# Kernel tuning notes

Hardware: AMD Instinct MI355X
Metric: run time of the kernel (lower is better)

## Reference

```python
import jax, jax.numpy as jnp
import numpy as np
import math

EPS = 1e-5  # BatchNorm eps; eval mode with running_mean=0, running_var=1


def maxpool(x, k, p):
    return jax.lax.reduce_window(x, -jnp.inf, jax.lax.max,
                                 (1, 1, k, k), (1, 1, 1, 1),
                                 ((0, 0), (0, 0), (p, p), (p, p)))


def conv1x1(x, w, b=None):
    # x: [B,Cin,H,W], w: [Cout,Cin]
    y = jnp.einsum('oi,bihw->bohw', w, x)
    if b is not None:
        y = y + b[None, :, None, None]
    return y


def bn_eval(x, g, b):
    scale = g / jnp.sqrt(1.0 + EPS)
    return x * scale[None, :, None, None] + b[None, :, None, None]


def setup_inputs() -> dict:
    B, C, H, W = 2, 64, 80, 80
    c1, c2, c3 = 21, 21, 22
    ch = 32  # C//2
    ks = jax.random.split(jax.random.key(0), 16)
    s = 0.05
    inp = {
        'x': jax.random.normal(ks[0], (B, C, H, W), jnp.float32),
        'q1_w': jax.random.normal(ks[1], (c1, c1), jnp.float32) * s,
        'q1_g': jnp.ones((c1,), jnp.float32),
        'q1_b': jnp.zeros((c1,), jnp.float32),
        'q2_w': jax.random.normal(ks[2], (c2, c2), jnp.float32) * s,
        'q2_g': jnp.ones((c2,), jnp.float32),
        'q2_b': jnp.zeros((c2,), jnp.float32),
        'q3_w': jax.random.normal(ks[3], (c3, c3), jnp.float32) * s,
        'q3_g': jnp.ones((c3,), jnp.float32),
        'q3_b': jnp.zeros((c3,), jnp.float32),
        'k_hf_w': jax.random.normal(ks[4], (ch, C), jnp.float32) * s,
        'k_hf_b': jnp.zeros((ch,), jnp.float32),
        'k_lf_w': jax.random.normal(ks[5], (C - ch, C), jnp.float32) * s,
        'k_lf_b': jnp.zeros((C - ch,), jnp.float32),
        'k_fuse_w': jax.random.normal(ks[6], (C, C), jnp.float32) * s,
        'k_fuse_b': jnp.zeros((C,), jnp.float32),
        'v_bn_g': jnp.ones((C,), jnp.float32),
        'v_bn_b': jnp.zeros((C,), jnp.float32),
        'v_w': jax.random.normal(ks[7], (C, C), jnp.float32) * s,
        'v_b': jnp.zeros((C,), jnp.float32),
        'out_w': jax.random.normal(ks[8], (C, C), jnp.float32) * s,
        'out_b': jnp.zeros((C,), jnp.float32),
    }
    return inp


def reference(x, q1_w, q1_g, q1_b, q2_w, q2_g, q2_b, q3_w, q3_g, q3_b,
              k_hf_w, k_hf_b, k_lf_w, k_lf_b, k_fuse_w, k_fuse_b,
              v_bn_g, v_bn_b, v_w, v_b, out_w, out_b):
    B, C, H, W = x.shape
    N = H * W
    c1 = q1_w.shape[0]
    c2 = q2_w.shape[0]
    # Q: ThreeGroupConvQ (split -> 1x1 conv (no bias) -> BN -> ReLU -> concat)
    x1, x2, x3 = jnp.split(x, [c1, c1 + c2], axis=1)
    y1 = jax.nn.relu(bn_eval(conv1x1(x1, q1_w), q1_g, q1_b))
    y2 = jax.nn.relu(bn_eval(conv1x1(x2, q2_w), q2_g, q2_b))
    y3 = jax.nn.relu(bn_eval(conv1x1(x3, q3_w), q3_g, q3_b))
    Q = jnp.concatenate([y1, y2, y3], axis=1)
    # K: ThermalStructureExtractor
    p3 = maxpool(x, 3, 1)
    p5 = maxpool(x, 5, 2)
    low = (p3 + p5) * 0.5
    high = conv1x1(x - low, k_hf_w, k_hf_b)
    lowp = conv1x1(low, k_lf_w, k_lf_b)
    K = conv1x1(jnp.concatenate([high, lowp], axis=1), k_fuse_w, k_fuse_b)
    # V: BN -> 1x1 conv
    V = conv1x1(bn_eval(x, v_bn_g, v_bn_b), v_w, v_b)
    # attention over N = H*W spatial tokens, channel features
    Qc = Q.reshape(B, C, N)
    Kc = K.reshape(B, C, N)
    Vc = V.reshape(B, C, N)
    attn = jax.nn.softmax(
        jnp.einsum('bcn,bcm->bnm', Qc, Kc) / math.sqrt(C), axis=-1)  # [B,N,N]
    out = jnp.einsum('bnm,bcm->bcn', attn, Vc).reshape(B, C, H, W)
    return conv1x1(out, out_w, out_b) + x
```

## Files before the change

### kernel.cpp

```cpp
#include <hip/hip_runtime.h>
#include <hip/hip_bf16.h>


#define BATCH 2
#define CH 64
#define HH 80
#define WW 80
#define NN 6400
#define NT 100
#define KS 10
#define KTPS (NT/KS)
#define EPSV 1e-5f
#define NEGBIG (-1e30f)
#define LOG2E8 0.18033688f
#define VSP 65

typedef __hip_bfloat16 bf16;
typedef __attribute__((ext_vector_type(8))) short short8;
typedef __attribute__((ext_vector_type(4))) float f4;
#define MFMA16 __builtin_amdgcn_mfma_f32_16x16x32_bf16

__device__ __forceinline__ float b2f(bf16 v){ return __bfloat162float(v); }
__device__ __forceinline__ bf16 f2b(float v){ return __float2bfloat16(v); }
__device__ __forceinline__ ushort f2bu(float v){ return ((__hip_bfloat16_raw)__float2bfloat16(v)).x; }
__device__ __forceinline__ float bu2f(ushort u){
  union { unsigned int i; float f; } w; w.i = ((unsigned int)u) << 16; return w.f;
}
__device__ __forceinline__ unsigned pkbf(float a, float b){
  union { __hip_bfloat162 h2; unsigned u; } cv;
  cv.h2 = __float22bfloat162_rn(make_float2(a, b));
  return cv.u;
}
__device__ __forceinline__ float fexp2(float x){
#if __has_builtin(__builtin_amdgcn_exp2f)
  return __builtin_amdgcn_exp2f(x);
#else
  return exp2f(x);
#endif
}
__device__ __forceinline__ int swz(int row, int colb){
  return row*128 + (colb ^ ((row & 7) << 4));
}

#define OFF_BIAS 0
#define OFF_WH_B 768
#define OFF_LOW_B (768 + 32768)
#define OFF_Q_B   (OFF_LOW_B + BATCH*CH*NN*2)
#define OFF_K_B   (OFF_Q_B   + BATCH*CH*NN*2)
#define OFF_V_B   (OFF_K_B   + BATCH*CH*NN*2)
#define OFF_P_B   (OFF_V_B   + BATCH*CH*NN*2)
#define OFF_ML_B  (OFF_P_B   + BATCH*NT*KS*4096*2)

__global__ __launch_bounds__(256) void setup_fold(
    const float* __restrict__ q1w, const float* __restrict__ q1g, const float* __restrict__ q1b,
    const float* __restrict__ q2w, const float* __restrict__ q2g, const float* __restrict__ q2b,
    const float* __restrict__ q3w, const float* __restrict__ q3g, const float* __restrict__ q3b,
    const float* __restrict__ khw, const float* __restrict__ khb,
    const float* __restrict__ klw, const float* __restrict__ klb,
    const float* __restrict__ kfw, const float* __restrict__ kfb,
    const float* __restrict__ vg,  const float* __restrict__ vbnb,
    const float* __restrict__ vw,  const float* __restrict__ vb,
    const float* __restrict__ outw,
    float* __restrict__ biasf, bf16* __restrict__ wh)
{
  __shared__ __align__(16) float skf[4096];
  __shared__ __align__(16) float skh[2048];
  __shared__ __align__(16) float skl[2048];
  __shared__ __align__(16) float sow[4096];
  __shared__ __align__(16) float svw[4096];
  __shared__ float sbv[64];

  int tid = threadIdx.x;
  int blk = blockIdx.x;
  #pragma unroll
  for (int i = 0; i < 4; ++i) {
    *(float4*)&skf[(i*256 + tid)*4] = *(const float4*)&kfw[(i*256 + tid)*4];
    *(float4*)&sow[(i*256 + tid)*4] = *(const float4*)&outw[(i*256 + tid)*4];
    *(float4*)&svw[(i*256 + tid)*4] = *(const float4*)&vw[(i*256 + tid)*4];
  }
  #pragma unroll
  for (int i = 0; i < 2; ++i) {
    *(float4*)&skh[(i*256 + tid)*4] = *(const float4*)&khw[(i*256 + tid)*4];
    *(float4*)&skl[(i*256 + tid)*4] = *(const float4*)&klw[(i*256 + tid)*4];
  }
  __syncthreads();

  float rs = rsqrtf(1.0f + EPSV);
  if (tid < 64) {
    int j = tid;
    float bvo = vb[j];
    for (int ci2 = 0; ci2 < 64; ++ci2) bvo += svw[j*64 + ci2] * vbnb[ci2];
    sbv[j] = bvo;
  }

  bf16* wq   = wh;
  bf16* wvp  = wh + 4096;
  bf16* wa1  = wh + 8192;
  bf16* wa2m = wh + 12288;

  int t = blk*256 + tid;
  int ci = t & 63, co = t >> 6;
  int o = ci*64 + co;

  float w = 0.f, g;
  if (co < 21)      { g = q1g[co];    w = (ci < 21)              ? q1w[co*21 + ci]            : 0.f; }
  else if (co < 42) { g = q2g[co-21]; w = (ci >= 21 && ci < 42)  ? q2w[(co-21)*21 + (ci-21)]  : 0.f; }
  else              { g = q3g[co-42]; w = (ci >= 42)             ? q3w[(co-42)*22 + (ci-42)]  : 0.f; }
  wq[o] = f2b(w * g * rs * LOG2E8);

  float a1 = 0.f, a2 = 0.f;
  #pragma unroll
  for (int j = 0; j < 32; ++j) {
    a1 += skf[co*64 + j]      * skh[j*64 + ci];
    a2 += skf[co*64 + 32 + j] * skl[j*64 + ci];
  }
  wa1[o]  = f2b(a1);
  wa2m[o] = f2b(a2 - a1);

  float av = 0.f;
  #pragma unroll
  for (int j = 0; j < 64; ++j)
    av += sow[co*64 + j] * svw[j*64 + ci];
  wvp[o] = f2b(av * vg[ci] * rs);

  if (blk == 0 && tid < 64) {
    int c2 = tid;
    float bq;
    if (c2 < 21)      bq = q1b[c2];
    else if (c2 < 42) bq = q2b[c2-21];
    else              bq = q3b[c2-42];
    biasf[c2] = bq * LOG2E8;
    float bk = kfb[c2];
    #pragma unroll
    for (int j = 0; j < 32; ++j) {
      bk += skf[c2*64 + j]      * khb[j];
      bk += skf[c2*64 + 32 + j] * klb[j];
    }
    biasf[64 + c2] = bk;
    float bvp = 0.f;
    #pragma unroll
    for (int j = 0; j < 64; ++j) bvp += sow[c2*64 + j] * sbv[j];
    biasf[128 + c2] = bvp;
  }
}

__global__ __launch_bounds__(256) void pool_low(const float* __restrict__ x,
                                                bf16* __restrict__ lowg)
{
  int t4 = (blockIdx.x*256 + threadIdx.x)*4;
  int bc = t4 / NN; int n = t4 % NN;
  int h = n / WW, w0 = n % WW;
  const float* p = x + bc*NN;
  float m5[4], m3[4];
  #pragma unroll
  for (int j=0;j<4;++j){ m5[j]=NEGBIG; m3[j]=NEGBIG; }
  #pragma unroll
  for (int dh = -2; dh <= 2; ++dh) {
    int hh = h + dh; if (hh < 0 || hh >= HH) continue;
    float r[12];
    const float* row = p + hh*WW;
    if (w0 >= 4)      { float4 a = *(const float4*)&row[w0-4]; r[0]=a.x;r[1]=a.y;r[2]=a.z;r[3]=a.w; }
    else              { r[0]=NEGBIG;r[1]=NEGBIG;r[2]=NEGBIG;r[3]=NEGBIG; }
    { float4 a = *(const float4*)&row[w0]; r[4]=a.x;r[5]=a.y;r[6]=a.z;r[7]=a.w; }
    if (w0 + 7 < WW)  { float4 a = *(const float4*)&row[w0+4]; r[8]=a.x;r[9]=a.y;r[10]=a.z;r[11]=a.w; }
    else              { r[8]=NEGBIG;r[9]=NEGBIG;r[10]=NEGBIG;r[11]=NEGBIG; }
    bool in3 = (dh >= -1 && dh <= 1);
    #pragma unroll
    for (int j=0;j<4;++j) {
      float v3 = fmaxf(fmaxf(r[3+j], r[4+j]), r[5+j]);
      float v5 = fmaxf(fmaxf(r[2+j], v3), r[6+j]);
      m5[j] = fmaxf(m5[j], v5);
      if (in3) m3[j] = fmaxf(m3[j], v3);
    }
  }
  ushort4 o;
  o.x = f2bu(0.5f*(m3[0]+m5[0]));
  o.y = f2bu(0.5f*(m3[1]+m5[1]));
  o.z = f2bu(0.5f*(m3[2]+m5[2]));
  o.w = f2bu(0.5f*(m3[3]+m5[3]));
  *(ushort4*)&lowg[t4] = o;
}

__global__ __launch_bounds__(256) void qkv_kernel(
    const float* __restrict__ x, const float* __restrict__ biasf,
    const bf16* __restrict__ wh, const bf16* __restrict__ lowg,
    bf16* __restrict__ qgT, bf16* __restrict__ kgT, bf16* __restrict__ vgc)
{
  __shared__ __align__(16) float xs[64*32];
  __shared__ __align__(16) float lows[64*32];
  __shared__ __align__(16) bf16  wbuf[16384];
  __shared__ ushort vs[64*VSP];
  __shared__ float bias[192];

  int tid = threadIdx.x;
  int blk = blockIdx.x;
  int b = blk / (NT*2);
  int rem = blk % (NT*2);
  int tile = rem >> 1, half = rem & 1;
  int n0 = tile*64 + half*32;

  #pragma unroll
  for (int i = 0; i < 8; ++i) {
    int e = i*256 + tid; int c = e >> 5, p = e & 31;
    xs[c*32 + p]   = x[(b*CH + c)*NN + n0 + p];
    lows[c*32 + p] = b2f(lowg[(b*CH + c)*NN + n0 + p]);
  }
  #pragma unroll
  for (int i = 0; i < 16; ++i)
    ((uint2*)wbuf)[i*256 + tid] = ((const uint2*)wh)[i*256 + tid];
  if (tid < 192) bias[tid] = biasf[tid];
  __syncthreads();

  int co = tid & 63, pg = tid >> 6;
  const bf16* wq   = wbuf;
  const bf16* wvp  = wbuf + 4096;
  const bf16* wa1  = wbuf + 8192;
  const bf16* wa2m = wbuf + 12288;

  {
    float bq = bias[co];
    float4 a0 = make_float4(bq,bq,bq,bq), a1v = a0;
    for (int ci = 0; ci < 64; ++ci) {
      float wv = b2f(wq[ci*64 + co]);
      float4 x0 = *(const float4*)&xs[ci*32 + pg*8];
      float4 x1 = *(const float4*)&xs[ci*32 + pg*8 + 4];
      a0.x += wv*x0.x; a0.y += wv*x0.y; a0.z += wv*x0.z; a0.w += wv*x0.w;
      a1v.x += wv*x1.x; a1v.y += wv*x1.y; a1v.z += wv*x1.z; a1v.w += wv*x1.w;
    }
    float q8[8] = {a0.x,a0.y,a0.z,a0.w,a1v.x,a1v.y,a1v.z,a1v.w};
    #pragma unroll
    for (int j=0;j<8;++j)
      qgT[(size_t)(b*NN + n0 + pg*8 + j)*64 + co] = f2b(fmaxf(q8[j], 0.f));
  }
  {
    float bv = bias[128 + co];
    float4 a0 = make_float4(bv,bv,bv,bv), a1v = a0;
    for (int ci = 0; ci < 64; ++ci) {
      float wv = b2f(wvp[ci*64 + co]);
      float4 x0 = *(const float4*)&xs[ci*32 + pg*8];
      float4 x1 = *(const float4*)&xs[ci*32 + pg*8 + 4];
      a0.x += wv*x0.x; a0.y += wv*x0.y; a0.z += wv*x0.z; a0.w += wv*x0.w;
      a1v.x += wv*x1.x; a1v.y += wv*x1.y; a1v.z += wv*x1.z; a1v.w += wv*x1.w;
    }
    float v8[8] = {a0.x,a0.y,a0.z,a0.w,a1v.x,a1v.y,a1v.z,a1v.w};
    #pragma unroll
    for (int j=0;j<8;++j)
      vs[co*VSP + pg*8 + j] = f2bu(v8[j]);
  }
  __syncthreads();
  {
    int c = tid >> 2, cb = (tid & 3)*8;
    ushort u[8];
    #pragma unroll
    for (int j=0;j<8;++j) u[j] = vs[c*VSP + cb + j];
    uint4 pk;
    pk.x = (uint)u[0] | ((uint)u[1] << 16);
    pk.y = (uint)u[2] | ((uint)u[3] << 16);
    pk.z = (uint)u[4] | ((uint)u[5] << 16);
    pk.w = (uint)u[6] | ((uint)u[7] << 16);
    *(uint4*)&vgc[(size_t)(b*CH + c)*NN + n0 + cb] = pk;
  }
  {
    float bk = bias[64 + co];
    float4 a0 = make_float4(bk,bk,bk,bk), a1v = a0;
    for (int ci = 0; ci < 64; ++ci) {
      float w1 = b2f(wa1[ci*64 + co]);
      float w2 = b2f(wa2m[ci*64 + co]);
      float4 x0 = *(const float4*)&xs[ci*32 + pg*8];
      float4 x1 = *(const float4*)&xs[ci*32 + pg*8 + 4];
      float4 l0 = *(const float4*)&lows[ci*32 + pg*8];
      float4 l1 = *(const float4*)&lows[ci*32 + pg*8 + 4];
      a0.x += w1*x0.x + w2*l0.x; a0.y += w1*x0.y + w2*l0.y;
      a0.z += w1*x0.z + w2*l0.z; a0.w += w1*x0.w + w2*l0.w;
      a1v.x += w1*x1.x + w2*l1.x; a1v.y += w1*x1.y + w2*l1.y;
      a1v.z += w1*x1.z + w2*l1.z; a1v.w += w1*x1.w + w2*l1.w;
    }
    float k8[8] = {a0.x,a0.y,a0.z,a0.w,a1v.x,a1v.y,a1v.z,a1v.w};
    #pragma unroll
    for (int j=0;j<8;++j)
      kgT[(size_t)(b*NN + n0 + pg*8 + j)*64 + co] = f2b(k8[j]);
  }
}

__global__ __launch_bounds__(256, 2) void attn_partial(
    const bf16* __restrict__ qgT, const bf16* __restrict__ kgT, const bf16* __restrict__ vgc,
    ushort* __restrict__ part, float* __restrict__ pml)
{
  __shared__ __align__(16) char smem[32768];
  __shared__ float lred[256];

  int tid = threadIdx.x;
  int blk = blockIdx.x;
  int b = blk / (NT*KS);
  int rem = blk % (NT*KS);
  int tile = rem / KS, split = rem % KS;
  int n0 = tile*64;
  int wv = tid >> 6, lane = tid & 63, ln = lane & 15, quad = lane >> 4;
  int mbase = split*KTPS*64;

  int r0 = tid >> 3,         c0 = (tid & 7)*8;
  int r1 = 32 + (tid >> 3),  c1 = (tid & 7)*8;

  {
    uint4 qa = *(const uint4*)&qgT[(size_t)(b*NN + n0 + r0)*64 + c0];
    uint4 qb = *(const uint4*)&qgT[(size_t)(b*NN + n0 + r1)*64 + c1];
    *(uint4*)(smem + swz(r0, c0*2)) = qa;
    *(uint4*)(smem + swz(r1, c1*2)) = qb;
  }
  __syncthreads();
  short8 bq00 = *(const short8*)(smem + swz( 0*16 + ln, quad*16));
  short8 bq01 = *(const short8*)(smem + swz( 0*16 + ln, 64 + quad*16));
  short8 bq10 = *(const short8*)(smem + swz( 1*16 + ln, quad*16));
  short8 bq11 = *(const short8*)(smem + swz( 1*16 + ln, 64 + quad*16));
  short8 bq20 = *(const short8*)(smem + swz( 2*16 + ln, quad*16));
  short8 bq21 = *(const short8*)(smem + swz( 2*16 + ln, 64 + quad*16));
  short8 bq30 = *(const short8*)(smem + swz( 3*16 + ln, quad*16));
  short8 bq31 = *(const short8*)(smem + swz( 3*16 + ln, 64 + quad*16));
  {
    uint4 va = *(const uint4*)&vgc[(size_t)(b*CH + r0)*NN + mbase + c0];
    uint4 vb4 = *(const uint4*)&vgc[(size_t)(b*CH + r1)*NN + mbase + c1];
    *(uint4*)(smem + 16384 + swz(r0, c0*2)) = va;
    *(uint4*)(smem + 16384 + swz(r1, c1*2)) = vb4;
  }
  const bf16* kb = kgT + (size_t)(b*NN + mbase + wv*16 + ln)*64;
  short8 ak0 = *(const short8*)&kb[quad*8];
  short8 ak1 = *(const short8*)&kb[32 + quad*8];
  __syncthreads();

  f4 accO0 = (f4){0.f,0.f,0.f,0.f};
  f4 accO1 = (f4){0.f,0.f,0.f,0.f};
  f4 accO2 = (f4){0.f,0.f,0.f,0.f};
  f4 accO3 = (f4){0.f,0.f,0.f,0.f};
  float lacc0 = 0.f, lacc1 = 0.f, lacc2 = 0.f, lacc3 = 0.f;

  uint4 vr0, vr1;
  short8 an0, an1;
  for (int kt = 0; kt < KTPS; ++kt) {
    const int po = (kt & 1) * 8192;
    const int vo = 16384 + (kt & 1) * 8192;
    {
      int ktn = (kt + 1 < KTPS) ? kt + 1 : kt;
      int m1 = mbase + ktn*64;
      vr0 = *(const uint4*)&vgc[(size_t)(b*CH + r0)*NN + m1 + c0];
      vr1 = *(const uint4*)&vgc[(size_t)(b*CH + r1)*NN + m1 + c1];
      an0 = *(const short8*)&kb[(size_t)ktn*4096 + quad*8];
      an1 = *(const short8*)&kb[(size_t)ktn*4096 + 32 + quad*8];
    }

    f4 accS0, accS1, accS2, accS3;
    {
      f4 z = (f4){0.f,0.f,0.f,0.f};
      z = MFMA16(ak0, bq00, z, 0, 0, 0);
      accS0 = MFMA16(ak1, bq01, z, 0, 0, 0);
    }
    {
      f4 z = (f4){0.f,0.f,0.f,0.f};
      z = MFMA16(ak0, bq10, z, 0, 0, 0);
      accS1 = MFMA16(ak1, bq11, z, 0, 0, 0);
    }
    {
      f4 z = (f4){0.f,0.f,0.f,0.f};
      z = MFMA16(ak0, bq20, z, 0, 0, 0);
      accS2 = MFMA16(ak1, bq21, z, 0, 0, 0);
    }
    {
      f4 z = (f4){0.f,0.f,0.f,0.f};
      z = MFMA16(ak0, bq30, z, 0, 0, 0);
      accS3 = MFMA16(ak1, bq31, z, 0, 0, 0);
    }
    {
      float p0 = fexp2(accS0[0]), p1 = fexp2(accS0[1]);
      float p2 = fexp2(accS0[2]), p3 = fexp2(accS0[3]);
      lacc0 += (p0 + p1) + (p2 + p3);
      uint2 pk; pk.x = pkbf(p0, p1); pk.y = pkbf(p2, p3);
      *(uint2*)(smem + po + swz(0*16 + ln, wv*32 + quad*8)) = pk;
    }
    {
      float p0 = fexp2(accS1[0]), p1 = fexp2(accS1[1]);
      float p2 = fexp2(accS1[2]), p3 = fexp2(accS1[3]);
      lacc1 += (p0 + p1) + (p2 + p3);
      uint2 pk; pk.x = pkbf(p0, p1); pk.y = pkbf(p2, p3);
      *(uint2*)(smem + po + swz(1*16 + ln, wv*32 + quad*8)) = pk;
    }
    {
      float p0 = fexp2(accS2[0]), p1 = fexp2(accS2[1]);
      float p2 = fexp2(accS2[2]), p3 = fexp2(accS2[3]);
      lacc2 += (p0 + p1) + (p2 + p3);
      uint2 pk; pk.x = pkbf(p0, p1); pk.y = pkbf(p2, p3);
      *(uint2*)(smem + po + swz(2*16 + ln, wv*32 + quad*8)) = pk;
    }
    {
      float p0 = fexp2(accS3[0]), p1 = fexp2(accS3[1]);
      float p2 = fexp2(accS3[2]), p3 = fexp2(accS3[3]);
      lacc3 += (p0 + p1) + (p2 + p3);
      uint2 pk; pk.x = pkbf(p0, p1); pk.y = pkbf(p2, p3);
      *(uint2*)(smem + po + swz(3*16 + ln, wv*32 + quad*8)) = pk;
    }
    __syncthreads();

    short8 ap0 = *(const short8*)(smem + po + swz(wv*16 + ln, quad*16));
    short8 ap1 = *(const short8*)(smem + po + swz(wv*16 + ln, 64 + quad*16));
    {
      short8 bv0 = *(const short8*)(smem + vo + swz(0*16 + ln, quad*16));
      short8 bv1 = *(const short8*)(smem + vo + swz(0*16 + ln, 64 + quad*16));
      accO0 = MFMA16(ap0, bv0, accO0, 0, 0, 0);
      accO0 = MFMA16(ap1, bv1, accO0, 0, 0, 0);
    }
    {
      short8 bv0 = *(const short8*)(smem + vo + swz(1*16 + ln, quad*16));
      short8 bv1 = *(const short8*)(smem + vo + swz(1*16 + ln, 64 + quad*16));
      accO1 = MFMA16(ap0, bv0, accO1, 0, 0, 0);
      accO1 = MFMA16(ap1, bv1, accO1, 0, 0, 0);
    }
    {
      short8 bv0 = *(const short8*)(smem + vo + swz(2*16 + ln, quad*16));
      short8 bv1 = *(const short8*)(smem + vo + swz(2*16 + ln, 64 + quad*16));
      accO2 = MFMA16(ap0, bv0, accO2, 0, 0, 0);
      accO2 = MFMA16(ap1, bv1, accO2, 0, 0, 0);
    }
    {
      short8 bv0 = *(const short8*)(smem + vo + swz(3*16 + ln, quad*16));
      short8 bv1 = *(const short8*)(smem + vo + swz(3*16 + ln, 64 + quad*16));
      accO3 = MFMA16(ap0, bv0, accO3, 0, 0, 0);
      accO3 = MFMA16(ap1, bv1, accO3, 0, 0, 0);
    }
    if (kt + 1 < KTPS) {
      int vn = 16384 + ((kt+1) & 1) * 8192;
      *(uint4*)(smem + vn + swz(r0, c0*2)) = vr0;
      *(uint4*)(smem + vn + swz(r1, c1*2)) = vr1;
    }
    ak0 = an0; ak1 = an1;
  }

  size_t pbase = ((size_t)(b*NT + tile)*KS + split)*4096;
  ushort* pp = part + pbase;
  {
    uint2 pk; pk.x = pkbf(accO0[0], accO0[1]); pk.y = pkbf(accO0[2], accO0[3]);
    *(uint2*)&pp[(0*16 + ln)*64 + wv*16 + quad*4] = pk;
  }
  {
    uint2 pk; pk.x = pkbf(accO1[0], accO1[1]); pk.y = pkbf(accO1[2], accO1[3]);
    *(uint2*)&pp[(1*16 + ln)*64 + wv*16 + quad*4] = pk;
  }
  {
    uint2 pk; pk.x = pkbf(accO2[0], accO2[1]); pk.y = pkbf(accO2[2], accO2[3]);
    *(uint2*)&pp[(2*16 + ln)*64 + wv*16 + quad*4] = pk;
  }
  {
    uint2 pk; pk.x = pkbf(accO3[0], accO3[1]); pk.y = pkbf(accO3[2], accO3[3]);
    *(uint2*)&pp[(3*16 + ln)*64 + wv*16 + quad*4] = pk;
  }
  {
    float s = lacc0;
    s += __shfl_xor(s, 16); s += __shfl_xor(s, 32);
    if (quad == 0) lred[wv*64 + 0*16 + ln] = s;
  }
  {
    float s = lacc1;
    s += __shfl_xor(s, 16); s += __shfl_xor(s, 32);
    if (quad == 0) lred[wv*64 + 1*16 + ln] = s;
  }
  {
    float s = lacc2;
    s += __shfl_xor(s, 16); s += __shfl_xor(s, 32);
    if (quad == 0) lred[wv*64 + 2*16 + ln] = s;
  }
  {
    float s = lacc3;
    s += __shfl_xor(s, 16); s += __shfl_xor(s, 32);
    if (quad == 0) lred[wv*64 + 3*16 + ln] = s;
  }
  __syncthreads();
  if (tid < 64) {
    size_t mlb = ((size_t)(b*NT + tile)*KS + split)*64;
    pml[mlb + tid] = (lred[tid] + lred[64 + tid]) + (lred[128 + tid] + lred[192 + tid]);
  }
}

__global__ __launch_bounds__(256) void attn_reduce(
    const ushort* __restrict__ part, const float* __restrict__ pml,
    const float* __restrict__ x, const float* __restrict__ outb,
    float* __restrict__ out)
{
  __shared__ float linv[64];
  __shared__ float ob[64];

  int tid = threadIdx.x;
  int blk = blockIdx.x;
  int b = blk / NT, tile = blk % NT;
  size_t base = (size_t)(b*NT + tile)*KS;

  if (tid < 64) {
    float l = 0.f;
    #pragma unroll
    for (int s=0;s<KS;++s) l += pml[(base+s)*64 + tid];
    linv[tid] = 1.0f / l;
    ob[tid] = outb[tid];
  }
  __syncthreads();

  #pragma unroll
  for (int j = 0; j < 4; ++j) {
    int idx = j*256 + tid;
    int c = idx >> 4, q = idx & 15;
    float a0=0.f, a1=0.f, a2=0.f, a3=0.f;
    #pragma unroll
    for (int s = 0; s < KS; ++s) {
      uint2 v = *(const uint2*)&part[(base+s)*4096 + (size_t)c*64 + q*4];
      a0 += bu2f((ushort)(v.x & 0xffff)); a1 += bu2f((ushort)(v.x >> 16));
      a2 += bu2f((ushort)(v.y & 0xffff)); a3 += bu2f((ushort)(v.y >> 16));
    }
    int nl = q*4;
    size_t gidx = (size_t)(b*CH + c)*NN + tile*64 + nl;
    float4 xv = *(const float4*)&x[gidx];
    float bc = ob[c];
    float4 o;
    o.x = a0*linv[nl+0] + bc + xv.x;
    o.y = a1*linv[nl+1] + bc + xv.y;
    o.z = a2*linv[nl+2] + bc + xv.z;
    o.w = a3*linv[nl+3] + bc + xv.w;
    *(float4*)&out[gidx] = o;
  }
}

extern "C" void kernel_launch(void* const* d_in, const int* in_sizes, int n_in,
                              void* d_out, int out_size, void* d_ws, size_t ws_size,
                              hipStream_t stream) {
  const float* x    = (const float*)d_in[0];
  const float* q1w  = (const float*)d_in[1];
  const float* q1g  = (const float*)d_in[2];
  const float* q1b  = (const float*)d_in[3];
  const float* q2w  = (const float*)d_in[4];
  const float* q2g  = (const float*)d_in[5];
  const float* q2b  = (const float*)d_in[6];
  const float* q3w  = (const float*)d_in[7];
  const float* q3g  = (const float*)d_in[8];
  const float* q3b  = (const float*)d_in[9];
  const float* khw  = (const float*)d_in[10];
  const float* khb  = (const float*)d_in[11];
  const float* klw  = (const float*)d_in[12];
  const float* klb  = (const float*)d_in[13];
  const float* kfw  = (const float*)d_in[14];
  const float* kfb  = (const float*)d_in[15];
  const float* vbg  = (const float*)d_in[16];
  const float* vbb  = (const float*)d_in[17];
  const float* vw   = (const float*)d_in[18];
  const float* vb   = (const float*)d_in[19];
  const float* outw = (const float*)d_in[20];
  const float* outb = (const float*)d_in[21];

  char*   wsb  = (char*)d_ws;
  float*  biasf= (float*)(wsb + OFF_BIAS);
  bf16*   wh   = (bf16*)(wsb + OFF_WH_B);
  bf16*   lowg = (bf16*)(wsb + OFF_LOW_B);
  bf16*   qgT  = (bf16*)(wsb + OFF_Q_B);
  bf16*   kgT  = (bf16*)(wsb + OFF_K_B);
  bf16*   vgc  = (bf16*)(wsb + OFF_V_B);
  ushort* part = (ushort*)(wsb + OFF_P_B);
  float*  pml  = (float*)(wsb + OFF_ML_B);

  hipLaunchKernelGGL(setup_fold, dim3(16), dim3(256), 0, stream,
                     q1w,q1g,q1b,q2w,q2g,q2b,q3w,q3g,q3b,
                     khw,khb,klw,klb,kfw,kfb,vbg,vbb,vw,vb,outw, biasf, wh);
  hipLaunchKernelGGL(pool_low, dim3(BATCH*CH*NN/1024), dim3(256), 0, stream, x, lowg);
  hipLaunchKernelGGL(qkv_kernel, dim3(BATCH*NT*2), dim3(256), 0, stream,
                     x, biasf, wh, lowg, qgT, kgT, vgc);
  hipLaunchKernelGGL(attn_partial, dim3(BATCH*NT*KS), dim3(256), 0, stream,
                     qgT, kgT, vgc, part, pml);
  hipLaunchKernelGGL(attn_reduce, dim3(BATCH*NT), dim3(256), 0, stream,
                     part, pml, x, outb, (float*)d_out);
}
```

Before: 160.1 us.

## Load V operands directly from global memory and halve key splits

The attention partial kernel no longer stages V tiles through double-buffered shared memory. Each lane now reads its MFMA B-operand fragments for V straight from global memory (or L2), which halves LDS usage and removes the LDS stores and reads for V. The split count drops from 10 to 5, so each block walks twice as many key tiles and fewer partials have to be combined. The trade-off is that the global V loads sit on the critical path without explicit prefetch, fewer blocks are launched, and the launch-bound occupancy may be affected.

```diff
diff --git a/kernel.cpp b/kernel.cpp
--- a/kernel.cpp
+++ b/kernel.cpp
@@ -8,7 +8,7 @@
 #define WW 80
 #define NN 6400
 #define NT 100
-#define KS 10
+#define KS 5
 #define KTPS (NT/KS)
 #define EPSV 1e-5f
 #define NEGBIG (-1e30f)
@@ -286,7 +286,7 @@
     const bf16* __restrict__ qgT, const bf16* __restrict__ kgT, const bf16* __restrict__ vgc,
     ushort* __restrict__ part, float* __restrict__ pml)
 {
-  __shared__ __align__(16) char smem[32768];
+  __shared__ __align__(16) char smem[16384];
   __shared__ float lred[256];
 
   int tid = threadIdx.x;
@@ -316,15 +316,10 @@
   short8 bq21 = *(const short8*)(smem + swz( 2*16 + ln, 64 + quad*16));
   short8 bq30 = *(const short8*)(smem + swz( 3*16 + ln, quad*16));
   short8 bq31 = *(const short8*)(smem + swz( 3*16 + ln, 64 + quad*16));
-  {
-    uint4 va = *(const uint4*)&vgc[(size_t)(b*CH + r0)*NN + mbase + c0];
-    uint4 vb4 = *(const uint4*)&vgc[(size_t)(b*CH + r1)*NN + mbase + c1];
-    *(uint4*)(smem + 16384 + swz(r0, c0*2)) = va;
-    *(uint4*)(smem + 16384 + swz(r1, c1*2)) = vb4;
-  }
   const bf16* kb = kgT + (size_t)(b*NN + mbase + wv*16 + ln)*64;
   short8 ak0 = *(const short8*)&kb[quad*8];
   short8 ak1 = *(const short8*)&kb[32 + quad*8];
+  const bf16* vB = vgc + ((size_t)b*CH + ln)*NN + mbase + quad*8;
   __syncthreads();
 
   f4 accO0 = (f4){0.f,0.f,0.f,0.f};
@@ -333,16 +328,11 @@
   f4 accO3 = (f4){0.f,0.f,0.f,0.f};
   float lacc0 = 0.f, lacc1 = 0.f, lacc2 = 0.f, lacc3 = 0.f;
 
-  uint4 vr0, vr1;
   short8 an0, an1;
   for (int kt = 0; kt < KTPS; ++kt) {
     const int po = (kt & 1) * 8192;
-    const int vo = 16384 + (kt & 1) * 8192;
     {
       int ktn = (kt + 1 < KTPS) ? kt + 1 : kt;
-      int m1 = mbase + ktn*64;
-      vr0 = *(const uint4*)&vgc[(size_t)(b*CH + r0)*NN + m1 + c0];
-      vr1 = *(const uint4*)&vgc[(size_t)(b*CH + r1)*NN + m1 + c1];
       an0 = *(const short8*)&kb[(size_t)ktn*4096 + quad*8];
       an1 = *(const short8*)&kb[(size_t)ktn*4096 + 32 + quad*8];
     }
@@ -400,34 +390,30 @@
 
     short8 ap0 = *(const short8*)(smem + po + swz(wv*16 + ln, quad*16));
     short8 ap1 = *(const short8*)(smem + po + swz(wv*16 + ln, 64 + quad*16));
-    {
-      short8 bv0 = *(const short8*)(smem + vo + swz(0*16 + ln, quad*16));
-      short8 bv1 = *(const short8*)(smem + vo + swz(0*16 + ln, 64 + quad*16));
+    const bf16* vk = vB + kt*64;
+    {
+      short8 bv0 = *(const short8*)&vk[(size_t)(0*16)*NN];
+      short8 bv1 = *(const short8*)&vk[(size_t)(0*16)*NN + 32];
       accO0 = MFMA16(ap0, bv0, accO0, 0, 0, 0);
       accO0 = MFMA16(ap1, bv1, accO0, 0, 0, 0);
     }
     {
-      short8 bv0 = *(const short8*)(smem + vo + swz(1*16 + ln, quad*16));
-      short8 bv1 = *(const short8*)(smem + vo + swz(1*16 + ln, 64 + quad*16));
+      short8 bv0 = *(const short8*)&vk[(size_t)(1*16)*NN];
+      short8 bv1 = *(const short8*)&vk[(size_t)(1*16)*NN + 32];
       accO1 = MFMA16(ap0, bv0, accO1, 0, 0, 0);
       accO1 = MFMA16(ap1, bv1, accO1, 0, 0, 0);
     }
     {
-      short8 bv0 = *(const short8*)(smem + vo + swz(2*16 + ln, quad*16));
-      short8 bv1 = *(const short8*)(smem + vo + swz(2*16 + ln, 64 + quad*16));
+      short8 bv0 = *(const short8*)&vk[(size_t)(2*16)*NN];
+      short8 bv1 = *(const short8*)&vk[(size_t)(2*16)*NN + 32];
       accO2 = MFMA16(ap0, bv0, accO2, 0, 0, 0);
       accO2 = MFMA16(ap1, bv1, accO2, 0, 0, 0);
     }
     {
-      short8 bv0 = *(const short8*)(smem + vo + swz(3*16 + ln, quad*16));
-      short8 bv1 = *(const short8*)(smem + vo + swz(3*16 + ln, 64 + quad*16));
+      short8 bv0 = *(const short8*)&vk[(size_t)(3*16)*NN];
+      short8 bv1 = *(const short8*)&vk[(size_t)(3*16)*NN + 32];
       accO3 = MFMA16(ap0, bv0, accO3, 0, 0, 0);
       accO3 = MFMA16(ap1, bv1, accO3, 0, 0, 0);
-    }
-    if (kt + 1 < KTPS) {
-      int vn = 16384 + ((kt+1) & 1) * 8192;
-      *(uint4*)(smem + vn + swz(r0, c0*2)) = vr0;
-      *(uint4*)(smem + vn + swz(r1, c1*2)) = vr1;
     }
     ak0 = an0; ak1 = an1;
   }
```

Measured after the change: 216.2 us. +35.1%, slower.
